# Kernel optimization log

Measured on AMD Instinct MI355X. Metric: run time of the kernel, lower is better.

## Reference

```python
import jax, jax.numpy as jnp
import numpy as np

PAD_ID, BOS_ID, EOS_ID = 0, 2, 3
NHEAD = 8


def _sincos(T, d):
    pos = jnp.arange(T, dtype=jnp.float32)
    omega = jnp.exp(-jnp.arange(0, d, 2, dtype=jnp.float32) * (np.log(10000.0) / d))
    out = pos[:, None] * omega[None, :]  # [T, d/2]
    return jnp.stack([jnp.sin(out), jnp.cos(out)], axis=2).reshape(T, d)[None]  # [1,T,d]


def _ln(x, g, b, eps=1e-5):
    mu = x.mean(-1, keepdims=True)
    var = ((x - mu) ** 2).mean(-1, keepdims=True)
    return (x - mu) / jnp.sqrt(var + eps) * g + b


def _mha(q_in, kv_in, wqkv, bqkv, wo, bo, mask):
    B, Tq, d = q_in.shape
    Tk = kv_in.shape[1]
    hd = d // NHEAD
    q = q_in @ wqkv[:d].T + bqkv[:d]
    k = kv_in @ wqkv[d:2 * d].T + bqkv[d:2 * d]
    v = kv_in @ wqkv[2 * d:].T + bqkv[2 * d:]
    q = q.reshape(B, Tq, NHEAD, hd).transpose(0, 2, 1, 3)
    k = k.reshape(B, Tk, NHEAD, hd).transpose(0, 2, 1, 3)
    v = v.reshape(B, Tk, NHEAD, hd).transpose(0, 2, 1, 3)
    s = jnp.einsum('bhqd,bhkd->bhqk', q, k) / np.sqrt(hd)
    if mask is not None:
        s = s + mask
    a = jax.nn.softmax(s, axis=-1)
    o = jnp.einsum('bhqk,bhkd->bhqd', a, v).transpose(0, 2, 1, 3).reshape(B, Tq, d)
    return o @ wo.T + bo


def _last_logits(tokens, state, emb_table, qkv_w, qkv_b, out_w, out_b,
                 ffn_w1, ffn_b1, ffn_w2, ffn_b2, ln_g, ln_b):
    T = tokens.shape[1]
    d = emb_table.shape[1]
    x = emb_table[tokens] * np.sqrt(d) + _sincos(T, d)
    mask = jnp.where(jnp.tril(jnp.ones((T, T), bool)), 0.0, -jnp.inf)
    L = qkv_w.shape[0]
    for l in range(L):
        x = _ln(x + _mha(x, x, qkv_w[l, 0], qkv_b[l, 0], out_w[l, 0], out_b[l, 0], mask), ln_g[l, 0], ln_b[l, 0])
        x = _ln(x + _mha(x, state, qkv_w[l, 1], qkv_b[l, 1], out_w[l, 1], out_b[l, 1], None), ln_g[l, 1], ln_b[l, 1])
        h = jax.nn.gelu(x @ ffn_w1[l].T + ffn_b1[l], approximate=False)
        x = _ln(x + h @ ffn_w2[l].T + ffn_b2[l], ln_g[l, 2], ln_b[l, 2])
    return x[:, -1, :] @ emb_table.T  # tied output projection


def setup_inputs() -> dict:
    key = jax.random.key(0)
    ks = jax.random.split(key, 8)
    V, d, L, dff, B, K = 32000, 512, 4, 2048, 8, 64
    s = 0.02
    emb = jax.random.normal(ks[1], (V, d), jnp.float32) * s
    emb = emb.at[PAD_ID].set(0.0)  # padding_idx row is zero
    return {
        'state': jax.random.normal(ks[0], (B, K, d), jnp.float32),
        'emb_table': emb,
        'qkv_w': jax.random.normal(ks[2], (L, 2, 3 * d, d), jnp.float32) * s,
        'qkv_b': jnp.zeros((L, 2, 3 * d), jnp.float32),
        'out_w': jax.random.normal(ks[3], (L, 2, d, d), jnp.float32) * s,
        'out_b': jnp.zeros((L, 2, d), jnp.float32),
        'ffn_w1': jax.random.normal(ks[4], (L, dff, d), jnp.float32) * s,
        'ffn_b1': jnp.zeros((L, dff), jnp.float32),
        'ffn_w2': jax.random.normal(ks[5], (L, d, dff), jnp.float32) * s,
        'ffn_b2': jnp.zeros((L, d), jnp.float32),
        'ln_g': jnp.ones((L, 3, d), jnp.float32),
        'ln_b': jnp.zeros((L, 3, d), jnp.float32),
        'max_length': 16,
        'top_k': 50,
    }


def reference(state, emb_table, qkv_w, qkv_b, out_w, out_b, ffn_w1, ffn_b1,
              ffn_w2, ffn_b2, ln_g, ln_b, max_length, top_k):
    B = state.shape[0]
    generated = jnp.full((B, 1), BOS_ID, dtype=jnp.int32)
    finished = jnp.zeros(B, dtype=bool)
    key = jax.random.key(1)
    temperature = 1.0
    for t in range(max_length):
        # faithful naive recompute: full self+cross attention over generated prefix
        logits = _last_logits(generated, state, emb_table, qkv_w, qkv_b, out_w, out_b,
                              ffn_w1, ffn_b1, ffn_w2, ffn_b2, ln_g, ln_b)
        logits = logits / max(temperature, 1e-8)
        thr = jax.lax.top_k(logits, top_k)[0][:, -1:]
        filt = jnp.where(logits < thr, -jnp.inf, logits)
        nxt = jax.random.categorical(jax.random.fold_in(key, t), filt, axis=-1)
        nxt = jnp.where(finished, PAD_ID, nxt).astype(jnp.int32)
        generated = jnp.concatenate([generated, nxt[:, None]], axis=1)
        finished = finished | (nxt == EOS_ID)
    return generated
```

## Files before the change

### kernel.cpp

```cpp
#include <hip/hip_runtime.h>
#include <math.h>
#include <stdint.h>

#define D     512
#define DFF   2048
#define BB    8
#define NB    2
#define NG    4
#define NH    8
#define HD    64
#define NV    32000
#define NL    4
#define TMAX  17
#define KC    64
#define STEPS 16
#define KTOP  50
#define PAD_ID 0
#define BOS_ID 2
#define EOS_ID 3
#define SCOPE __HIP_MEMORY_SCOPE_AGENT

__device__ __forceinline__ float ld1(const float* p) {
  return __hip_atomic_load(p, __ATOMIC_RELAXED, SCOPE);
}
__device__ __forceinline__ void st1(float* p, float v) {
  __hip_atomic_store(p, v, __ATOMIC_RELAXED, SCOPE);
}
__device__ __forceinline__ float2 ld2(const float* p) {
  union { double d; float2 f; } u;
  u.d = __hip_atomic_load((const double*)p, __ATOMIC_RELAXED, SCOPE);
  return u.f;
}
__device__ __forceinline__ unsigned ldu(const unsigned* p) {
  return __hip_atomic_load(p, __ATOMIC_RELAXED, SCOPE);
}

__device__ __forceinline__ void tf2x32(unsigned k0, unsigned k1, unsigned x0, unsigned x1,
                                       unsigned& o0, unsigned& o1)
{
  unsigned ks2 = k0 ^ k1 ^ 0x1BD11BDAu;
#define TFR(r) { x0 += x1; x1 = (x1 << (r)) | (x1 >> (32 - (r))); x1 ^= x0; }
  x0 += k0; x1 += k1;
  TFR(13) TFR(15) TFR(26) TFR(6)
  x0 += k1;  x1 += ks2 + 1u;
  TFR(17) TFR(29) TFR(16) TFR(24)
  x0 += ks2; x1 += k0 + 2u;
  TFR(13) TFR(15) TFR(26) TFR(6)
  x0 += k0;  x1 += k1 + 3u;
  TFR(17) TFR(29) TFR(16) TFR(24)
  x0 += k1;  x1 += ks2 + 4u;
  TFR(13) TFR(15) TFR(26) TFR(6)
  o0 = x0 + ks2; o1 = x1 + k0 + 5u;
#undef TFR
}

__device__ __forceinline__ float wredf(float v) {
  for (int o = 32; o; o >>= 1) v += __shfl_xor(v, o, 64);
  return v;
}
__device__ __forceinline__ float wredmaxf(float v) {
  for (int o = 32; o; o >>= 1) v = fmaxf(v, __shfl_xor(v, o, 64));
  return v;
}
__device__ __forceinline__ unsigned monok(float f) {
  unsigned u = __float_as_uint(f);
  return (u & 0x80000000u) ? ~u : (u | 0x80000000u);
}

#define DOT8(a0,a1,x0,x1) (a0.x*x0.x + a0.y*x0.y + a0.z*x0.z + a0.w*x0.w + \
                           a1.x*x1.x + a1.y*x1.y + a1.z*x1.z + a1.w*x1.w)

__global__ void init_k(int* toks, unsigned* bars)
{
  int i = threadIdx.x;
  if (i < BB) toks[i * TMAX] = BOS_ID;
  for (int k = i; k < 2048; k += 256) bars[k] = 0u;
}

__global__ void cross_kv_k(const float* __restrict__ state, const float* __restrict__ qkvw,
                           const float* __restrict__ qkvb, float* __restrict__ cK,
                           float* __restrict__ cV)
{
  int gx = blockIdx.x, b = blockIdx.y, tid = threadIdx.x;
  int jblk = gx & 31, kpos = (gx >> 5) & 63, l = gx >> 11;
  int w = tid >> 6, lane = tid & 63;
  __shared__ __align__(16) float xsh[D];
  xsh[tid] = state[((size_t)b * KC + kpos) * D + tid];
  xsh[tid + 256] = state[((size_t)b * KC + kpos) * D + tid + 256];
  __syncthreads();
  for (int i = 0; i < 8; i++) {
    int j = jblk * 32 + w * 8 + i;
    int row = D + j;
    const float4* wr = (const float4*)(qkvw + (((size_t)l * 2 + 1) * (3 * D) + row) * D);
    const float4* x4 = (const float4*)xsh;
    float acc = 0.f;
    for (int e = lane; e < 128; e += 64) {
      float4 a = wr[e], xx = x4[e];
      acc += a.x * xx.x + a.y * xx.y + a.z * xx.z + a.w * xx.w;
    }
    acc = wredf(acc);
    if (lane == 0) {
      float v = acc + qkvb[((size_t)l * 2 + 1) * (3 * D) + row];
      float* dst = (j < D) ? cK : cV;
      int jj = (j < D) ? j : j - D;
      dst[(((size_t)l * BB + b) * KC + kpos) * D + jj] = v;
    }
  }
}

extern "C" __global__ void __launch_bounds__(512, 2)
decode_k(const float* __restrict__ emb, const float* __restrict__ qkv_w,
         const float* __restrict__ qkv_b, const float* __restrict__ out_w,
         const float* __restrict__ out_b, const float* __restrict__ f_w1,
         const float* __restrict__ f_b1, const float* __restrict__ f_w2,
         const float* __restrict__ f_b2, const float* __restrict__ lng,
         const float* __restrict__ lnb,
         const float* __restrict__ cK, const float* __restrict__ cV,
         float* Kc, float* Vc, float* qS, float* q2S,
         float* xt2, float* xt3, float* xt4, float* hB,
         float* xcur, float* lg, unsigned* bars, int* toks)
{
  const int tid = threadIdx.x, bid = blockIdx.x;
  const int xcd = bid & 7;
  const int g2 = xcd >> 1;
  const int half = xcd & 1;
  const int hid = bid >> 3;
  const int gid = hid * 2 + half;
  const int sb = (gid + g2 * 16) & 63;
  const int b0 = g2 * 2, b1 = b0 + 1;
  const int w = tid >> 6, lane = tid & 63;
  const int wb = w >> 2;
  const int ws = w & 3;
  unsigned gp = 0, glp = 0;
  int finished = 0;

  __shared__ __align__(16) unsigned char smem[65280];
  float* F = (float*)smem;
  float* sX1 = F;
  float* sX2 = F + 1024;
  float* sQ  = F + 2048;
  float* sAO = F + 3072;
  float* sS  = F + 4096;
  float* sSP = F + 5184;
  float* sH  = F + 6272;
  float* sRed = F + 10368;
  float* sL  = F;
  unsigned short* key16 = (unsigned short*)smem;
  unsigned* histA = (unsigned*)(smem + 64000);
  unsigned* sKeys = (unsigned*)(smem + 64000);
  unsigned* sMeta = (unsigned*)(smem + 65024);
  float*    sWin  = (float*)(smem + 65056);
  int*      sWix  = (int*)(smem + 65120);

  const float SQD = (float)22.627416997969522;
  const float PEC = (float)(9.210340371976184 / 512.0);
  const float SQRT2 = (float)1.4142135623730951;

  auto gbarg = [&]() {
    asm volatile("s_waitcnt vmcnt(0)" ::: "memory");
    __syncthreads();
    ++gp;
    if (tid == 0) {
      unsigned* c = bars + g2 * 256;
      __hip_atomic_fetch_add(&c[(gid & 3) * 32], 1u, __ATOMIC_RELAXED, SCOPE);
      unsigned tgt = gp * 16u;
      for (;;) {
        unsigned s0 = ldu(&c[0]), s1 = ldu(&c[32]), s2 = ldu(&c[64]), s3 = ldu(&c[96]);
        unsigned mn = s0 < s1 ? s0 : s1;
        unsigned mn2 = s2 < s3 ? s2 : s3;
        if ((mn < mn2 ? mn : mn2) >= tgt) break;
        __builtin_amdgcn_s_sleep(1);
      }
    }
    asm volatile("" ::: "memory");
    __syncthreads();
  };
  auto gbarall = [&]() {
    asm volatile("s_waitcnt vmcnt(0)" ::: "memory");
    __syncthreads();
    ++glp;
    if (tid == 0) {
      unsigned* c = bars + 1024;
      __hip_atomic_fetch_add(&c[(bid & 15) * 32], 1u, __ATOMIC_RELAXED, SCOPE);
      unsigned tgt = glp * 16u;
      for (;;) {
        unsigned mn = 0xFFFFFFFFu;
#pragma unroll
        for (int i = 0; i < 16; i++) { unsigned x = ldu(&c[i * 32]); mn = x < mn ? x : mn; }
        if (mn >= tgt) break;
        __builtin_amdgcn_s_sleep(1);
      }
    }
    asm volatile("" ::: "memory");
    __syncthreads();
  };

  auto ln2 = [&](const float* srcbase, const float* gamma, const float* beta, float* dst) {
    int nb = tid >> 8, e = tid & 255;
    const float* sp = srcbase + (size_t)(b0 + nb) * D;
    float v0 = ld1(sp + e), v1 = ld1(sp + e + 256);
    float s = wredf(v0 + v1);
    if (lane == 0) sRed[w] = s;
    __syncthreads();
    float mu = (sRed[nb*4] + sRed[nb*4+1] + sRed[nb*4+2] + sRed[nb*4+3]) * (1.0f/512.0f);
    __syncthreads();
    float d0 = v0 - mu, d1 = v1 - mu;
    float q = wredf(d0*d0 + d1*d1);
    if (lane == 0) sRed[w] = q;
    __syncthreads();
    float sd = sqrtf((sRed[nb*4] + sRed[nb*4+1] + sRed[nb*4+2] + sRed[nb*4+3]) * (1.0f/512.0f) + 1e-5f);
    dst[nb*512 + e]       = d0 / sd * gamma[e]       + beta[e];
    dst[nb*512 + e + 256] = d1 / sd * gamma[e + 256] + beta[e + 256];
    __syncthreads();
  };

  if (bid < BB) {
    float pe = (tid & 1) ? 1.0f : 0.0f;
    st1(&xcur[bid * D + tid], emb[(size_t)BOS_ID * D + tid] * SQD + pe);
  }
  gbarg();

  for (int t = 0; t < STEPS; ++t) {
    const int T = t + 1;
    for (int l = 0; l < NL; ++l) {
      const float* wqkv0 = qkv_w + ((size_t)l * 2 + 0) * (3 * D) * D;
      const float* bqkv0 = qkv_b + ((size_t)l * 2 + 0) * (3 * D);
      const float* wqkv1 = qkv_w + ((size_t)l * 2 + 1) * (3 * D) * D;
      const float* bqkv1 = qkv_b + ((size_t)l * 2 + 1) * (3 * D);
      const float* wo0 = out_w + ((size_t)l * 2 + 0) * D * D;
      const float* bo0 = out_b + ((size_t)l * 2 + 0) * D;
      const float* wo1 = out_w + ((size_t)l * 2 + 1) * D * D;
      const float* bo1 = out_b + ((size_t)l * 2 + 1) * D;

      if (l == 0) {
        int nb = tid >> 8, e = tid & 255;
        sX1[nb*512 + e]       = ld1(&xcur[(b0 + nb) * D + e]);
        sX1[nb*512 + e + 256] = ld1(&xcur[(b0 + nb) * D + e + 256]);
        __syncthreads();
      } else {
        ln2(xt4, lng + ((size_t)(l - 1) * 3 + 2) * D, lnb + ((size_t)(l - 1) * 3 + 2) * D, sX1);
      }
      {
        const float4* xs4 = (const float4*)(sX1 + wb * 512);
        float4 x0 = xs4[lane], x1v = xs4[lane + 64];
        int jq = sb * 8 + ws * 2;
        int kvb = 512 + sb * 16 + ws * 4;
        float4 qa[2], qb[2], wa[4], wbv[4];
#pragma unroll
        for (int r = 0; r < 2; ++r) {
          const float4* w4 = (const float4*)(wqkv0 + (size_t)(jq + r) * D);
          qa[r] = w4[lane]; qb[r] = w4[lane + 64];
        }
#pragma unroll
        for (int r = 0; r < 4; ++r) {
          const float4* w4 = (const float4*)(wqkv0 + (size_t)(kvb + r) * D);
          wa[r] = w4[lane]; wbv[r] = w4[lane + 64];
        }
        float aq[2], ak[4];
#pragma unroll
        for (int r = 0; r < 2; ++r) aq[r] = DOT8(qa[r], qb[r], x0, x1v);
#pragma unroll
        for (int r = 0; r < 4; ++r) ak[r] = DOT8(wa[r], wbv[r], x0, x1v);
#pragma unroll
        for (int o = 32; o; o >>= 1) {
#pragma unroll
          for (int r = 0; r < 2; ++r) aq[r] += __shfl_xor(aq[r], o, 64);
#pragma unroll
          for (int r = 0; r < 4; ++r) ak[r] += __shfl_xor(ak[r], o, 64);
        }
        if (lane == 0) {
#pragma unroll
          for (int r = 0; r < 2; ++r) {
            int j = jq + r;
            st1(&qS[(size_t)(b0 + wb) * D + j], aq[r] + bqkv0[j]);
          }
#pragma unroll
          for (int r = 0; r < 4; ++r) {
            int j = kvb + r;
            float v = ak[r] + bqkv0[j];
            if (j < 1024)
              st1(&Kc[((((size_t)g2 * NL + l) * NB + wb) * TMAX + t) * D + (j - 512)], v);
            else
              st1(&Vc[((((size_t)g2 * NL + l) * NB + wb) * TMAX + t) * D + (j - 1024)], v);
          }
        }
      }
      gbarg();

      {
        int nb = tid >> 8, e = tid & 255;
        sQ[nb*512 + e]       = ld1(&qS[(b0 + nb) * D + e]);
        sQ[nb*512 + e + 256] = ld1(&qS[(b0 + nb) * D + e + 256]);
      }
      __syncthreads();
      for (int o = tid; o < NB * NH * TMAX; o += 512) {
        int nb = o / (NH * TMAX), rem = o - nb * (NH * TMAX);
        int h = rem / TMAX, k = rem - h * TMAX;
        if (k < T) {
          const float4* Kr = (const float4*)(Kc + ((((size_t)g2 * NL + l) * NB + nb) * TMAX + k) * D + h * HD);
          const float4* q4 = (const float4*)(sQ + nb * 512 + h * HD);
          float sc = 0.f;
#pragma unroll
          for (int e = 0; e < 16; ++e) {
            float4 a = Kr[e], b2 = q4[e];
            sc += a.x * b2.x + a.y * b2.y + a.z * b2.z + a.w * b2.w;
          }
          sS[nb * 544 + h * TMAX + k] = sc * 0.125f;
        }
      }
      __syncthreads();
      for (int rr = w; rr < 16; rr += 8) {
        int nb = rr >> 3, h = rr & 7;
        float v = (lane < T) ? sS[nb * 544 + h * TMAX + lane] : -INFINITY;
        float m = wredmaxf(v);
        float p = (lane < T) ? expf(v - m) : 0.f;
        float den = wredf(p);
        if (lane < T) sSP[nb * 544 + h * TMAX + lane] = p / den;
      }
      __syncthreads();
      for (int o = tid; o < 1024; o += 512) {
        int nb = o >> 9, dd = o & 511, h = dd >> 6, d3 = dd & 63;
        const float* Vb = Vc + ((((size_t)g2 * NL + l) * NB + nb) * TMAX) * D + h * HD + d3;
        float acc = 0.f;
        for (int k = 0; k < T; ++k) acc += sSP[nb * 544 + h * TMAX + k] * Vb[(size_t)k * D];
        sAO[nb * 512 + dd] = acc;
      }
      __syncthreads();
      {
        int jb = sb * 8 + ws * 2;
        const float4* yN = (const float4*)(sAO + wb * 512);
        float4 y0 = yN[lane], y1 = yN[lane + 64];
        float acc[2];
#pragma unroll
        for (int r = 0; r < 2; ++r) {
          const float4* w4 = (const float4*)(wo0 + (size_t)(jb + r) * D);
          float4 a0 = w4[lane], a1 = w4[lane + 64];
          acc[r] = DOT8(a0, a1, y0, y1);
        }
#pragma unroll
        for (int o = 32; o; o >>= 1) {
#pragma unroll
          for (int r = 0; r < 2; ++r) acc[r] += __shfl_xor(acc[r], o, 64);
        }
        if (lane == 0) {
#pragma unroll
          for (int r = 0; r < 2; ++r) {
            int j = jb + r;
            st1(&xt2[(size_t)(b0 + wb) * D + j], acc[r] + bo0[j] + sX1[wb * 512 + j]);
          }
        }
      }
      gbarg();

      ln2(xt2, lng + ((size_t)l * 3 + 0) * D, lnb + ((size_t)l * 3 + 0) * D, sX2);
      {
        int jb = sb * 8 + ws * 2;
        const float4* yN = (const float4*)(sX2 + wb * 512);
        float4 y0 = yN[lane], y1 = yN[lane + 64];
        float acc[2];
#pragma unroll
        for (int r = 0; r < 2; ++r) {
          const float4* w4 = (const float4*)(wqkv1 + (size_t)(jb + r) * D);
          float4 a0 = w4[lane], a1 = w4[lane + 64];
          acc[r] = DOT8(a0, a1, y0, y1);
        }
#pragma unroll
        for (int o = 32; o; o >>= 1) {
#pragma unroll
          for (int r = 0; r < 2; ++r) acc[r] += __shfl_xor(acc[r], o, 64);
        }
        if (lane == 0) {
#pragma unroll
          for (int r = 0; r < 2; ++r) {
            int j = jb + r;
            st1(&q2S[(size_t)(b0 + wb) * D + j], acc[r] + bqkv1[j]);
          }
        }
      }
      gbarg();

      {
        int nb = tid >> 8, e = tid & 255;
        sQ[nb*512 + e]       = ld1(&q2S[(b0 + nb) * D + e]);
        sQ[nb*512 + e + 256] = ld1(&q2S[(b0 + nb) * D + e + 256]);
      }
      __syncthreads();
      for (int o = tid; o < 1024; o += 512) {
        int nb = o >> 9, dd = o & 511, h = dd >> 6, k = dd & 63;
        const float4* Kr = (const float4*)(cK + (((size_t)l * BB + b0 + nb) * KC + k) * D + h * HD);
        const float4* q4 = (const float4*)(sQ + nb * 512 + h * HD);
        float sc = 0.f;
#pragma unroll
        for (int e = 0; e < 16; ++e) {
          float4 a = Kr[e], b2 = q4[e];
          sc += a.x * b2.x + a.y * b2.y + a.z * b2.z + a.w * b2.w;
        }
        sS[nb * 512 + dd] = sc * 0.125f;
      }
      __syncthreads();
      for (int rr = w; rr < 16; rr += 8) {
        int nb = rr >> 3, h = rr & 7;
        float v = sS[nb * 512 + h * 64 + lane];
        float m = wredmaxf(v);
        float p = expf(v - m);
        float den = wredf(p);
        sSP[nb * 512 + h * 64 + lane] = p / den;
      }
      __syncthreads();
      for (int o = tid; o < 1024; o += 512) {
        int nb = o >> 9, dd = o & 511, h = dd >> 6, d3 = dd & 63;
        const float* Vb = cV + (((size_t)l * BB + b0 + nb) * KC) * D + h * HD + d3;
        float acc = 0.f;
        for (int k = 0; k < KC; ++k) acc += sSP[nb * 512 + h * 64 + k] * Vb[(size_t)k * D];
        sAO[nb * 512 + dd] = acc;
      }
      __syncthreads();
      {
        int jb = sb * 8 + ws * 2;
        const float4* yN = (const float4*)(sAO + wb * 512);
        float4 y0 = yN[lane], y1 = yN[lane + 64];
        float acc[2];
#pragma unroll
        for (int r = 0; r < 2; ++r) {
          const float4* w4 = (const float4*)(wo1 + (size_t)(jb + r) * D);
          float4 a0 = w4[lane], a1 = w4[lane + 64];
          acc[r] = DOT8(a0, a1, y0, y1);
        }
#pragma unroll
        for (int o = 32; o; o >>= 1) {
#pragma unroll
          for (int r = 0; r < 2; ++r) acc[r] += __shfl_xor(acc[r], o, 64);
        }
        if (lane == 0) {
#pragma unroll
          for (int r = 0; r < 2; ++r) {
            int j = jb + r;
            st1(&xt3[(size_t)(b0 + wb) * D + j], acc[r] + bo1[j] + sX2[wb * 512 + j]);
          }
        }
      }
      gbarg();

      ln2(xt3, lng + ((size_t)l * 3 + 1) * D, lnb + ((size_t)l * 3 + 1) * D, sX1);
      {
        const float4* xs4 = (const float4*)(sX1 + wb * 512);
        float4 x0 = xs4[lane], x1v = xs4[lane + 64];
        for (int pass = 0; pass < 2; ++pass) {
          int jb = sb * 32 + ws * 8 + pass * 4;
          float4 wa[4], wbv[4];
#pragma unroll
          for (int r = 0; r < 4; ++r) {
            const float4* w4 = (const float4*)(f_w1 + (size_t)l * DFF * D + (size_t)(jb + r) * D);
            wa[r] = w4[lane]; wbv[r] = w4[lane + 64];
          }
          float acc[4];
#pragma unroll
          for (int r = 0; r < 4; ++r) acc[r] = DOT8(wa[r], wbv[r], x0, x1v);
#pragma unroll
          for (int o = 32; o; o >>= 1) {
#pragma unroll
            for (int r = 0; r < 4; ++r) acc[r] += __shfl_xor(acc[r], o, 64);
          }
          if (lane == 0) {
#pragma unroll
            for (int r = 0; r < 4; ++r) {
              int j = jb + r;
              float v = acc[r] + f_b1[(size_t)l * DFF + j];
              v = v * (erff(v / SQRT2) + 1.0f) / 2.0f;
              st1(&hB[(size_t)(b0 + wb) * DFF + j], v);
            }
          }
        }
      }
      gbarg();

      for (int ii = tid; ii < 2048; ii += 512) {
        int nbb = ii >> 10, ee = (ii & 1023) * 2;
        float2 v = ld2(&hB[(size_t)(b0 + nbb) * DFF + ee]);
        sH[nbb * 2048 + ee] = v.x; sH[nbb * 2048 + ee + 1] = v.y;
      }
      __syncthreads();
      {
        int jb = sb * 8 + ws * 2;
        const float4* hN = (const float4*)(sH + wb * 2048);
        float acc[2];
#pragma unroll
        for (int r = 0; r < 2; ++r) {
          const float4* w4 = (const float4*)(f_w2 + (size_t)l * D * DFF + (size_t)(jb + r) * DFF);
          float a = 0.f;
#pragma unroll
          for (int e = 0; e < 8; ++e) {
            float4 aw0 = w4[lane + e * 64];
            float4 hh0 = hN[lane + e * 64];
            a += aw0.x * hh0.x + aw0.y * hh0.y + aw0.z * hh0.z + aw0.w * hh0.w;
          }
          acc[r] = a;
        }
#pragma unroll
        for (int o = 32; o; o >>= 1) {
#pragma unroll
          for (int r = 0; r < 2; ++r) acc[r] += __shfl_xor(acc[r], o, 64);
        }
        if (lane == 0) {
#pragma unroll
          for (int r = 0; r < 2; ++r) {
            int j = jb + r;
            st1(&xt4[(size_t)(b0 + wb) * D + j], acc[r] + f_b2[(size_t)l * D + j] + sX1[wb * 512 + j]);
          }
        }
      }
      if (l < NL - 1) gbarg(); else gbarall();
    }

    for (int ii = tid; ii < 2048; ii += 512) {
      float2 v = ld2(&xt4[2 * ii]);
      sL[2 * ii] = v.x; sL[2 * ii + 1] = v.y;
    }
    __syncthreads();
    {
      int b = w;
      float vals[8]; float s = 0.f;
#pragma unroll
      for (int e = 0; e < 8; ++e) { vals[e] = sL[b * D + lane + e * 64]; s += vals[e]; }
      s = wredf(s);
      float mu = s * (1.0f / 512.0f);
      float q = 0.f;
#pragma unroll
      for (int e = 0; e < 8; ++e) { float d0 = vals[e] - mu; q += d0 * d0; }
      q = wredf(q);
      float sd = sqrtf(q * (1.0f / 512.0f) + 1e-5f);
      const float* ga = lng + 11 * D;
      const float* be = lnb + 11 * D;
#pragma unroll
      for (int e = 0; e < 8; ++e)
        sL[b * D + lane + e * 64] = (vals[e] - mu) / sd * ga[lane + e * 64] + be[lane + e * 64];
    }
    __syncthreads();
    for (int i = w; i < 125; i += 8) {
      int v = i * 256 + bid;
      const float4* er = (const float4*)(emb + (size_t)v * D);
      float4 e0 = er[lane], e1 = er[lane + 64];
      float acc[8];
#pragma unroll
      for (int b = 0; b < 8; b++) {
        const float4* x4 = (const float4*)(sL + b * D);
        float4 x0 = x4[lane], x1v = x4[lane + 64];
        acc[b] = DOT8(e0, e1, x0, x1v);
      }
#pragma unroll
      for (int o = 32; o; o >>= 1) {
#pragma unroll
        for (int b = 0; b < 8; b++) acc[b] += __shfl_xor(acc[b], o, 64);
      }
      if (lane == 0) {
#pragma unroll
        for (int b = 0; b < 8; b++) st1(&lg[(size_t)b * NV + v], acc[b]);
      }
    }
    gbarall();

    if (bid < BB) {
      int b = bid;
      if (tid < 256) histA[tid] = 0u;
      __syncthreads();
      for (int v2 = tid; v2 < NV / 2; v2 += 512) {
        float2 f = ld2(&lg[(size_t)b * NV + 2 * v2]);
        unsigned u0 = monok(f.x), u1 = monok(f.y);
        key16[2 * v2] = (unsigned short)(u0 >> 16);
        key16[2 * v2 + 1] = (unsigned short)(u1 >> 16);
        atomicAdd(&histA[u0 >> 24], 1u);
        atomicAdd(&histA[u1 >> 24], 1u);
      }
      __syncthreads();
      if (tid == 0) {
        unsigned k = KTOP, cum = 0;
        for (int bin = 255; bin >= 0; bin--) {
          cum += histA[bin];
          if (cum >= k) { sMeta[0] = (unsigned)bin; sMeta[1] = k - (cum - histA[bin]); break; }
        }
      }
      __syncthreads();
      unsigned selHi = sMeta[0], rem1 = sMeta[1];
      if (tid < 256) histA[tid] = 0u;
      __syncthreads();
      for (int v = tid; v < NV; v += 512) {
        unsigned k16 = key16[v];
        if ((k16 >> 8) == selHi) atomicAdd(&histA[k16 & 255u], 1u);
      }
      __syncthreads();
      if (tid == 0) {
        unsigned k = rem1, cum = 0;
        for (int bin = 255; bin >= 0; bin--) {
          cum += histA[bin];
          if (cum >= k) { sMeta[2] = (selHi << 8) | (unsigned)bin; sMeta[1] = k - (cum - histA[bin]); break; }
        }
        sMeta[3] = 0u;
      }
      __syncthreads();
      unsigned P16 = sMeta[2], rem2 = sMeta[1];
      for (int v = tid; v < NV; v += 512) {
        if (key16[v] == (unsigned short)P16) {
          unsigned i = atomicAdd(&sMeta[3], 1u);
          if (i < 256) sKeys[i] = monok(ld1(&lg[(size_t)b * NV + v]));
        }
      }
      __syncthreads();
      if (tid == 0) {
        unsigned n = sMeta[3]; if (n > 256) n = 256;
        unsigned thr = 0;
        for (unsigned it = 0; it < rem2; ++it) {
          unsigned bestk = 0; int bj = 0;
          for (unsigned jx = 0; jx < n; jx++)
            if (sKeys[jx] > bestk) { bestk = sKeys[jx]; bj = (int)jx; }
          thr = bestk;
          sKeys[bj] = 0u;
        }
        sMeta[5] = (thr & 0x80000000u) ? (thr ^ 0x80000000u) : ~thr;
      }
      __syncthreads();
      float th = __uint_as_float(sMeta[5]);
      unsigned k0, k1;
      tf2x32(0u, 1u, 0u, (unsigned)t, k0, k1);
      float best = -INFINITY; int bi = NV;
      for (int v = tid; v < NV; v += 512) {
        if (key16[v] >= (unsigned short)P16) {
          float lo = ld1(&lg[(size_t)b * NV + v]);
          if (lo >= th) {
            unsigned o0, o1;
            tf2x32(k0, k1, 0u, (unsigned)(b * NV + v), o0, o1);
            unsigned bits = o0 ^ o1;
            unsigned ub = (bits >> 9) | 0x3f800000u;
            float fu = __uint_as_float(ub) - 1.0f;
            const float TINY = 1.17549435e-38f;
            float u = fu * (1.0f - TINY) + TINY;
            u = fmaxf(TINY, u);
            float gmb = -logf(-logf(u));
            float s = lo + gmb;
            if (s > best || (s == best && v < bi)) { best = s; bi = v; }
          }
        }
      }
      for (int o = 32; o; o >>= 1) {
        float ob = __shfl_xor(best, o, 64); int ox = __shfl_xor(bi, o, 64);
        if (ob > best || (ob == best && ox < bi)) { best = ob; bi = ox; }
      }
      if (lane == 0) { sWin[w] = best; sWix[w] = bi; }
      __syncthreads();
      if (tid == 0) {
        float bb = sWin[0]; int bx = sWix[0];
        for (int i2 = 1; i2 < 8; i2++) {
          if (sWin[i2] > bb || (sWin[i2] == bb && sWix[i2] < bx)) { bb = sWin[i2]; bx = sWix[i2]; }
        }
        int tok = bx;
        if (finished) tok = PAD_ID;
        toks[b * TMAX + t + 1] = tok;
        if (tok == EOS_ID) finished = 1;
        sMeta[4] = (unsigned)tok;
      }
      __syncthreads();
      {
        int tok = (int)sMeta[4];
        float omega = expf(-(float)(tid & ~1) * PEC);
        float val = (float)(t + 1) * omega;
        float pe = (tid & 1) ? cosf(val) : sinf(val);
        st1(&xcur[b * D + tid], emb[(size_t)tok * D + tid] * SQD + pe);
      }
    }
    gbarg();
  }
}

extern "C" void kernel_launch(void* const* d_in, const int* in_sizes, int n_in,
                              void* d_out, int out_size, void* d_ws, size_t ws_size,
                              hipStream_t stream)
{
  const float* state = (const float*)d_in[0];
  const float* emb   = (const float*)d_in[1];
  const float* qkv_w = (const float*)d_in[2];
  const float* qkv_b = (const float*)d_in[3];
  const float* out_w = (const float*)d_in[4];
  const float* out_b = (const float*)d_in[5];
  const float* f_w1  = (const float*)d_in[6];
  const float* f_b1  = (const float*)d_in[7];
  const float* f_w2  = (const float*)d_in[8];
  const float* f_b2  = (const float*)d_in[9];
  const float* lng   = (const float*)d_in[10];
  const float* lnb   = (const float*)d_in[11];

  float* ws = (float*)d_ws;
  float* cK   = ws;
  float* cV   = cK + (size_t)NL * BB * KC * D;
  float* Kc   = cV + (size_t)NL * BB * KC * D;
  float* Vc   = Kc + (size_t)8 * NL * NB * TMAX * D;
  float* qS   = Vc + (size_t)8 * NL * NB * TMAX * D;
  float* q2S  = qS + BB * D;
  float* xt2  = q2S + BB * D;
  float* xt3  = xt2 + BB * D;
  float* xt4  = xt3 + BB * D;
  float* hB   = xt4 + BB * D;
  float* xcur = hB + BB * DFF;
  float* lg   = xcur + BB * D;
  unsigned* bars = (unsigned*)(lg + (size_t)BB * NV);

  int* toks = (int*)d_out;

  init_k<<<1, 256, 0, stream>>>(toks, bars);
  cross_kv_k<<<dim3(NL * KC * 32, BB), 256, 0, stream>>>(state, qkv_w, qkv_b, cK, cV);
  decode_k<<<256, 512, 0, stream>>>(emb, qkv_w, qkv_b, out_w, out_b,
                                    f_w1, f_b1, f_w2, f_b2, lng, lnb,
                                    cK, cV, Kc, Vc, qS, q2S,
                                    xt2, xt3, xt4, hB, xcur, lg, bars, toks);
}
```

Baseline: 5.580 ms.

## Replace atomic-counter grid barriers with per-block flag slots and leader broadcast

Each block now stores its barrier epoch into its own padded flag slot instead of doing an atomic add on a shared counter. One leader block's first wavefront polls all slots in parallel and takes the minimum with a wave shuffle reduction. When every block has arrived, it writes broadcast flags that the other blocks spin on. This removes atomic contention and reduces the number of polling loads on shared lines, at the cost of an extra hop through the leader and a larger barrier buffer.

```diff
diff --git a/kernel.cpp b/kernel.cpp
--- a/kernel.cpp
+++ b/kernel.cpp
@@ -20,6 +20,12 @@
 #define EOS_ID 3
 #define SCOPE __HIP_MEMORY_SCOPE_AGENT
 
+#define BAR_GSLOT(g,i)  ((g) * 64 * 16 + (i) * 16)
+#define BAR_GBC(g,i)    (4096 + ((g) * 4 + (i)) * 16)
+#define BAR_ASLOT(i)    (4608 + (i) * 16)
+#define BAR_ABC(i)      (8704 + (i) * 16)
+#define BAR_TOTAL       16384
+
 __device__ __forceinline__ float ld1(const float* p) {
   return __hip_atomic_load(p, __ATOMIC_RELAXED, SCOPE);
 }
@@ -33,6 +39,9 @@
 }
 __device__ __forceinline__ unsigned ldu(const unsigned* p) {
   return __hip_atomic_load(p, __ATOMIC_RELAXED, SCOPE);
+}
+__device__ __forceinline__ void stu(unsigned* p, unsigned v) {
+  __hip_atomic_store(p, v, __ATOMIC_RELAXED, SCOPE);
 }
 
 __device__ __forceinline__ void tf2x32(unsigned k0, unsigned k1, unsigned x0, unsigned x1,
@@ -74,7 +83,7 @@
 {
   int i = threadIdx.x;
   if (i < BB) toks[i * TMAX] = BOS_ID;
-  for (int k = i; k < 2048; k += 256) bars[k] = 0u;
+  for (int k = i; k < BAR_TOTAL; k += 256) bars[k] = 0u;
 }
 
 __global__ void cross_kv_k(const float* __restrict__ state, const float* __restrict__ qkvw,
@@ -160,17 +169,23 @@
     asm volatile("s_waitcnt vmcnt(0)" ::: "memory");
     __syncthreads();
     ++gp;
-    if (tid == 0) {
-      unsigned* c = bars + g2 * 256;
-      __hip_atomic_fetch_add(&c[(gid & 3) * 32], 1u, __ATOMIC_RELAXED, SCOPE);
-      unsigned tgt = gp * 16u;
-      for (;;) {
-        unsigned s0 = ldu(&c[0]), s1 = ldu(&c[32]), s2 = ldu(&c[64]), s3 = ldu(&c[96]);
-        unsigned mn = s0 < s1 ? s0 : s1;
-        unsigned mn2 = s2 < s3 ? s2 : s3;
-        if ((mn < mn2 ? mn : mn2) >= tgt) break;
-        __builtin_amdgcn_s_sleep(1);
-      }
+    if (tid == 0) stu(&bars[BAR_GSLOT(g2, gid)], gp);
+    if (gid == 0) {
+      if (w == 0) {
+        for (;;) {
+          unsigned v = ldu(&bars[BAR_GSLOT(g2, lane)]);
+#pragma unroll
+          for (int o = 32; o; o >>= 1) {
+            unsigned x = __shfl_xor((int)v, o, 64);
+            v = x < v ? x : v;
+          }
+          if (v >= gp) break;
+          __builtin_amdgcn_s_sleep(1);
+        }
+        if (lane < 4) stu(&bars[BAR_GBC(g2, lane)], gp);
+      }
+    } else if (tid == 0) {
+      while (ldu(&bars[BAR_GBC(g2, gid & 3)]) < gp) __builtin_amdgcn_s_sleep(1);
     }
     asm volatile("" ::: "memory");
     __syncthreads();
@@ -179,17 +194,28 @@
     asm volatile("s_waitcnt vmcnt(0)" ::: "memory");
     __syncthreads();
     ++glp;
-    if (tid == 0) {
-      unsigned* c = bars + 1024;
-      __hip_atomic_fetch_add(&c[(bid & 15) * 32], 1u, __ATOMIC_RELAXED, SCOPE);
-      unsigned tgt = glp * 16u;
-      for (;;) {
-        unsigned mn = 0xFFFFFFFFu;
-#pragma unroll
-        for (int i = 0; i < 16; i++) { unsigned x = ldu(&c[i * 32]); mn = x < mn ? x : mn; }
-        if (mn >= tgt) break;
-        __builtin_amdgcn_s_sleep(1);
-      }
+    if (tid == 0) stu(&bars[BAR_ASLOT(bid)], glp);
+    if (bid == 0) {
+      if (w == 0) {
+        for (;;) {
+          unsigned mn = 0xFFFFFFFFu;
+#pragma unroll
+          for (int i = 0; i < 4; ++i) {
+            unsigned x = ldu(&bars[BAR_ASLOT(lane * 4 + i)]);
+            mn = x < mn ? x : mn;
+          }
+#pragma unroll
+          for (int o = 32; o; o >>= 1) {
+            unsigned x = __shfl_xor((int)mn, o, 64);
+            mn = x < mn ? x : mn;
+          }
+          if (mn >= glp) break;
+          __builtin_amdgcn_s_sleep(1);
+        }
+        if (lane < 16) stu(&bars[BAR_ABC(lane)], glp);
+      }
+    } else if (tid == 0) {
+      while (ldu(&bars[BAR_ABC(bid & 15)]) < glp) __builtin_amdgcn_s_sleep(1);
     }
     asm volatile("" ::: "memory");
     __syncthreads();
```

Result: faster. 5.110 ms (-8.4%).
